# Performance work log

Measured on AMD Instinct MI355X. Metric: run time of the kernel, lower is better.

The kernel has to match this reference:

```python
import jax, jax.numpy as jnp
import numpy as np

N = 50000
E = 800000
D = 256
C = 8
H = 64
LN_EPS = 1e-5


def setup_inputs() -> dict:
    key = jax.random.key(0)
    ks = jax.random.split(key, 8)
    x = jax.random.normal(ks[0], (N, D), dtype=jnp.float32)
    edge_index = jax.random.randint(ks[1], (2, E), 0, N, dtype=jnp.int64)
    omega = jax.random.uniform(ks[2], (E, C), dtype=jnp.float32)
    # xavier-uniform-ish parameter init
    def xavier(k, shape, fan_in, fan_out):
        a = float(np.sqrt(6.0 / (fan_in + fan_out)))
        return jax.random.uniform(k, shape, dtype=jnp.float32, minval=-a, maxval=a)
    proj = xavier(ks[3], (D, C, H), D, C * H)          # layer-0 projection
    W1 = xavier(ks[4], (C, H, H), H, H)                # layer-0 channel weights
    W2 = xavier(ks[5], (C, H, H), H, H)                # layer-1 channel weights
    ln_gamma = jnp.ones((H,), dtype=jnp.float32)
    ln_beta = jnp.zeros((H,), dtype=jnp.float32)
    return {"x": x, "edge_index": edge_index, "omega": omega,
            "proj": proj, "W1": W1, "W2": W2,
            "ln_gamma": ln_gamma, "ln_beta": ln_beta}


def _conv(h, src, dst, omega, W):
    # h: [N, C, H]; per-channel weighted scatter-add then channel-specific bmm.
    outs = []
    for c in range(C):  # small fixed channel loop, mirrors original structure
        msg = omega[:, c, None] * h[src, c, :]                  # [E, H]
        outs.append(jax.ops.segment_sum(msg, dst, num_segments=N))
    h_next = jnp.stack(outs, axis=1)                            # [N, C, H]
    return jnp.einsum('nch,cho->nco', h_next, W)                # channel bmm


def _layernorm(h, gamma, beta):
    mu = jnp.mean(h, axis=-1, keepdims=True)
    var = jnp.mean(jnp.square(h - mu), axis=-1, keepdims=True)
    return (h - mu) * jax.lax.rsqrt(var + LN_EPS) * gamma + beta


def reference(x, edge_index, omega, proj, W1, W2, ln_gamma, ln_beta):
    src, dst = edge_index[0], edge_index[1]
    # layer 0: project raw features into channel space [N, C, H]
    h = (x @ proj.reshape(D, C * H)).reshape(N, C, H)
    h = _conv(h, src, dst, omega, W1)
    h = _layernorm(h, ln_gamma, ln_beta)
    h = jax.nn.relu(h)
    # layer 1 (last layer: no ReLU)
    h = _conv(h, src, dst, omega, W2)
    h = _layernorm(h, ln_gamma, ln_beta)
    return h
```

## Files before the change

kernel.cpp:

```cpp
#include <hip/hip_runtime.h>

#define NN 50000
#define NE 800000
#define DD 256
#define CC 8
#define HH 64
#define CHW 512
#define LN_EPS 1e-5f
#define SCAN_BLOCKS ((NN + 1023) / 1024)

typedef __attribute__((ext_vector_type(8))) __bf16 bf16x8;
typedef __attribute__((ext_vector_type(4))) float f32x4;

__device__ inline ushort f2bf(float f) {
  uint u = __float_as_uint(f);
  return (ushort)((u + 0x7fffu + ((u >> 16) & 1u)) >> 16);
}

__device__ inline float om_decode(uint4 om, int c) {
  uint wd = (c & 2) ? ((c & 4) ? om.w : om.y) : ((c & 4) ? om.z : om.x);
  ushort hu = (c & 1) ? (ushort)(wd >> 16) : (ushort)(wd & 0xffffu);
  union { ushort u; _Float16 f; } cv; cv.u = hu;
  return (float)cv.f;
}

__device__ inline void acc8(float* acc, uint4 hv, float wt) {
  acc[0] += wt * __uint_as_float(hv.x << 16);
  acc[1] += wt * __uint_as_float(hv.x & 0xffff0000u);
  acc[2] += wt * __uint_as_float(hv.y << 16);
  acc[3] += wt * __uint_as_float(hv.y & 0xffff0000u);
  acc[4] += wt * __uint_as_float(hv.z << 16);
  acc[5] += wt * __uint_as_float(hv.z & 0xffff0000u);
  acc[6] += wt * __uint_as_float(hv.w << 16);
  acc[7] += wt * __uint_as_float(hv.w & 0xffff0000u);
}

__global__ __launch_bounds__(256) void fold_w1_kernel(
    const float* __restrict__ proj, const float* __restrict__ W1,
    ushort* __restrict__ projW1T) {
  __shared__ float wl[64];
  const int n = blockIdx.x;
  const int c = n >> 6, i = n & 63;
  const int tid = threadIdx.x;
  if (tid < 64) wl[tid] = W1[c * 4096 + tid * 64 + i];
  __syncthreads();
  const float* pr = proj + (size_t)tid * 512 + c * 64;
  float acc = 0.f;
#pragma unroll
  for (int k = 0; k < 64; ++k) acc += pr[k] * wl[k];
  projW1T[(size_t)n * 256 + tid] = f2bf(acc);
}

__global__ __launch_bounds__(256) void w2t_kernel(const float* __restrict__ W2,
                                                  ushort* __restrict__ W2T) {
  int c = blockIdx.x;
  for (int idx = threadIdx.x; idx < 4096; idx += 256) {
    int nn = idx >> 6, k = idx & 63;
    W2T[(size_t)c * 4096 + idx] = f2bf(W2[(size_t)c * 4096 + k * 64 + nn]);
  }
}

__global__ __launch_bounds__(256) void gemm_proj_kernel(
    const float* __restrict__ x, const ushort* __restrict__ BT,
    ushort* __restrict__ gout) {
  __shared__ ushort As[128 * 40];
  __shared__ ushort Bs[128 * 40];
  const int tid = threadIdx.x;
  const int lane = tid & 63, wv = tid >> 6;
  const int wm = wv >> 1, wn = wv & 1;
  const int lr = lane & 15, kg = lane >> 4;
  const int row0 = blockIdx.x * 128;
  const int col0 = blockIdx.y * 128;

  f32x4 acc[4][4];
#pragma unroll
  for (int i = 0; i < 4; ++i)
#pragma unroll
    for (int j = 0; j < 4; ++j) acc[i][j] = (f32x4){0.f, 0.f, 0.f, 0.f};

  for (int kk = 0; kk < 8; ++kk) {
    __syncthreads();
#pragma unroll
    for (int i = 0; i < 4; ++i) {
      int idx = tid + i * 256;
      int row = idx >> 3, quad = idx & 7;
      int rg = row0 + row;
      rg = rg < NN ? rg : NN - 1;
      float4 v = *(const float4*)(x + (size_t)rg * 256 + kk * 32 + quad * 4);
      ushort4 o = {f2bf(v.x), f2bf(v.y), f2bf(v.z), f2bf(v.w)};
      *(ushort4*)(As + row * 40 + quad * 4) = o;
    }
#pragma unroll
    for (int i = 0; i < 2; ++i) {
      int idx = tid + i * 256;
      int n = idx >> 2, quad = idx & 3;
      uint4 v = *(const uint4*)(BT + (size_t)(col0 + n) * 256 + kk * 32 + quad * 8);
      *(uint4*)(Bs + n * 40 + quad * 8) = v;
    }
    __syncthreads();
    bf16x8 a[4], b[4];
#pragma unroll
    for (int i = 0; i < 4; ++i)
      a[i] = *(const bf16x8*)(As + (wm * 64 + i * 16 + lr) * 40 + kg * 8);
#pragma unroll
    for (int j = 0; j < 4; ++j)
      b[j] = *(const bf16x8*)(Bs + (wn * 64 + j * 16 + lr) * 40 + kg * 8);
#pragma unroll
    for (int i = 0; i < 4; ++i)
#pragma unroll
      for (int j = 0; j < 4; ++j)
        acc[i][j] = __builtin_amdgcn_mfma_f32_16x16x32_bf16(a[i], b[j], acc[i][j], 0, 0, 0);
  }

  const int orow = kg * 4;
  const int ocol = lane & 15;
#pragma unroll
  for (int i = 0; i < 4; ++i) {
    int rg0 = row0 + wm * 64 + i * 16 + orow;
#pragma unroll
    for (int q = 0; q < 4; ++q) {
      int rg = rg0 + q;
      if (rg < NN) {
#pragma unroll
        for (int j = 0; j < 4; ++j) {
          gout[(size_t)rg * 512 + col0 + wn * 64 + j * 16 + ocol] = f2bf(acc[i][j][q]);
        }
      }
    }
  }
}

__global__ __launch_bounds__(256) void bmm_g_kernel(
    const ushort* __restrict__ h, const ushort* __restrict__ WT,
    ushort* __restrict__ g) {
  __shared__ ushort As[128 * 72];
  __shared__ ushort Bs[64 * 72];
  __shared__ float Cs[4][32 * 68];
  const int tid = threadIdx.x, lane = tid & 63, wv = tid >> 6;
  const int lr = lane & 15, kg = lane >> 4;
  const int n0 = blockIdx.x * 128;
  const int c = blockIdx.y;

#pragma unroll
  for (int i = 0; i < 4; ++i) {
    int idx = tid + i * 256;
    int row = idx >> 3, q = idx & 7;
    int rg = n0 + row;
    rg = rg < NN ? rg : NN - 1;
    *(uint4*)(As + row * 72 + q * 8) =
        *(const uint4*)(h + (size_t)rg * 512 + c * 64 + q * 8);
  }
#pragma unroll
  for (int i = 0; i < 2; ++i) {
    int idx = tid + i * 256;
    int row = idx >> 3, q = idx & 7;
    *(uint4*)(Bs + row * 72 + q * 8) =
        *(const uint4*)(WT + (size_t)c * 4096 + row * 64 + q * 8);
  }
  __syncthreads();

  f32x4 acc[2][4];
#pragma unroll
  for (int m = 0; m < 2; ++m)
#pragma unroll
    for (int j = 0; j < 4; ++j) acc[m][j] = (f32x4){0.f, 0.f, 0.f, 0.f};

#pragma unroll
  for (int ks = 0; ks < 2; ++ks) {
    bf16x8 a[2], b[4];
#pragma unroll
    for (int m = 0; m < 2; ++m)
      a[m] = *(const bf16x8*)(As + (wv * 32 + m * 16 + lr) * 72 + ks * 32 + kg * 8);
#pragma unroll
    for (int j = 0; j < 4; ++j)
      b[j] = *(const bf16x8*)(Bs + (j * 16 + lr) * 72 + ks * 32 + kg * 8);
#pragma unroll
    for (int m = 0; m < 2; ++m)
#pragma unroll
      for (int j = 0; j < 4; ++j)
        acc[m][j] = __builtin_amdgcn_mfma_f32_16x16x32_bf16(a[m], b[j], acc[m][j], 0, 0, 0);
  }

  float* cs = &Cs[wv][0];
#pragma unroll
  for (int m = 0; m < 2; ++m)
#pragma unroll
    for (int j = 0; j < 4; ++j)
#pragma unroll
      for (int q = 0; q < 4; ++q)
        cs[(m * 16 + kg * 4 + q) * 68 + j * 16 + lr] = acc[m][j][q];
  __syncthreads();

  const int row = lane & 31, half = lane >> 5;
  const int rg = n0 + wv * 32 + row;
  if (rg < NN) {
    const float* rp = cs + row * 68 + half * 32;
    ushort ob[32];
#pragma unroll
    for (int t = 0; t < 32; ++t) ob[t] = f2bf(rp[t]);
    ushort* op = g + (size_t)rg * 512 + c * 64 + half * 32;
#pragma unroll
    for (int t = 0; t < 4; ++t)
      *(uint4*)(op + t * 8) = *(uint4*)(ob + t * 8);
  }
}

__global__ void hist_kernel(const int* __restrict__ dst, int* __restrict__ cnt) {
  int e = blockIdx.x * 256 + threadIdx.x;
  if (e < NE) atomicAdd(&cnt[dst[e]], 1);
}

__global__ __launch_bounds__(1024) void scan1_kernel(const int* __restrict__ cnt,
                                                     int* __restrict__ blocksum) {
  __shared__ int ws[16];
  int tid = threadIdx.x, t = blockIdx.x * 1024 + tid;
  int v = (t < NN) ? cnt[t] : 0;
#pragma unroll
  for (int off = 32; off; off >>= 1) v += __shfl_xor(v, off);
  if ((tid & 63) == 0) ws[tid >> 6] = v;
  __syncthreads();
  if (tid < 16) {
    int s = ws[tid];
#pragma unroll
    for (int off = 8; off; off >>= 1) s += __shfl_xor(s, off, 16);
    if (tid == 0) blocksum[blockIdx.x] = s;
  }
}

__global__ __launch_bounds__(64) void scan2_kernel(int* __restrict__ blocksum,
                                                   int* __restrict__ rowptr) {
  int tid = threadIdx.x;
  int v = (tid < SCAN_BLOCKS) ? blocksum[tid] : 0;
  int orig = v;
#pragma unroll
  for (int off = 1; off < 64; off <<= 1) {
    int u = __shfl_up(v, off);
    if (tid >= off) v += u;
  }
  if (tid < SCAN_BLOCKS) blocksum[tid] = v - orig;
  if (tid == 63) rowptr[NN] = v;
}

__global__ __launch_bounds__(1024) void scan3_kernel(const int* __restrict__ blocksum,
                                                     int* __restrict__ cntcur,
                                                     int* __restrict__ rowptr) {
  __shared__ int ws[16];
  int tid = threadIdx.x, lane = tid & 63, wv = tid >> 6;
  int t = blockIdx.x * 1024 + tid;
  int orig = (t < NN) ? cntcur[t] : 0;
  int v = orig;
#pragma unroll
  for (int off = 1; off < 64; off <<= 1) {
    int u = __shfl_up(v, off);
    if (lane >= off) v += u;
  }
  if (lane == 63) ws[wv] = v;
  __syncthreads();
  if (tid < 16) {
    int s = ws[tid];
#pragma unroll
    for (int off = 1; off < 16; off <<= 1) {
      int u = __shfl_up(s, off, 16);
      if (tid >= off) s += u;
    }
    ws[tid] = s;
  }
  __syncthreads();
  if (t < NN) {
    int excl = blocksum[blockIdx.x] + (wv ? ws[wv - 1] : 0) + (v - orig);
    rowptr[t] = excl;
    cntcur[t] = excl;
  }
}

__global__ void fill_kernel(const int* __restrict__ dst, const int* __restrict__ src,
                            const float* __restrict__ omega, int* __restrict__ cursor,
                            int* __restrict__ esrc, uint4* __restrict__ eom) {
  int e = blockIdx.x * 256 + threadIdx.x;
  if (e < NE) {
    int d = dst[e];
    int pos = atomicAdd(&cursor[d], 1);
    esrc[pos] = src[e];
    const float4* om4 = (const float4*)(omega + (size_t)e * 8);
    float4 o0 = om4[0], o1 = om4[1];
    union { _Float16 f[8]; uint4 v; } pk;
    pk.f[0] = (_Float16)o0.x; pk.f[1] = (_Float16)o0.y;
    pk.f[2] = (_Float16)o0.z; pk.f[3] = (_Float16)o0.w;
    pk.f[4] = (_Float16)o1.x; pk.f[5] = (_Float16)o1.y;
    pk.f[6] = (_Float16)o1.z; pk.f[7] = (_Float16)o1.w;
    eom[pos] = pk.v;
  }
}

template <bool RELU, bool BF16OUT>
__global__ __launch_bounds__(256) void conv_ln_kernel(
    const ushort* __restrict__ g, const int* __restrict__ esrc,
    const uint4* __restrict__ eom, const int* __restrict__ rowptr,
    const float* __restrict__ gamma, const float* __restrict__ beta,
    void* __restrict__ outv) {
  int n = blockIdx.x * 4 + (threadIdx.x >> 6);
  if (n >= NN) return;
  const int lane = threadIdx.x & 63;
  const int c = lane >> 3;
  const int i0 = (lane & 7) * 8;
  int start = rowptr[n], end = rowptr[n + 1];
  const uint4* g4 = (const uint4*)g;
  float acc[8] = {0.f, 0.f, 0.f, 0.f, 0.f, 0.f, 0.f, 0.f};

  int idx = start;
  for (; idx + 3 < end; idx += 4) {
    int s0 = esrc[idx], s1 = esrc[idx + 1], s2 = esrc[idx + 2], s3 = esrc[idx + 3];
    uint4 om0 = eom[idx], om1 = eom[idx + 1], om2 = eom[idx + 2], om3 = eom[idx + 3];
    uint4 h0 = g4[(size_t)s0 * 64 + lane];
    uint4 h1 = g4[(size_t)s1 * 64 + lane];
    uint4 h2 = g4[(size_t)s2 * 64 + lane];
    uint4 h3 = g4[(size_t)s3 * 64 + lane];
    float w0 = om_decode(om0, c), w1 = om_decode(om1, c);
    float w2 = om_decode(om2, c), w3 = om_decode(om3, c);
    acc8(acc, h0, w0);
    acc8(acc, h1, w1);
    acc8(acc, h2, w2);
    acc8(acc, h3, w3);
  }
  for (; idx < end; ++idx) {
    int s = esrc[idx];
    uint4 om = eom[idx];
    uint4 hv = g4[(size_t)s * 64 + lane];
    acc8(acc, hv, om_decode(om, c));
  }

  float s8 = ((acc[0] + acc[1]) + (acc[2] + acc[3])) +
             ((acc[4] + acc[5]) + (acc[6] + acc[7]));
  s8 += __shfl_xor(s8, 1);
  s8 += __shfl_xor(s8, 2);
  s8 += __shfl_xor(s8, 4);
  float mu = s8 * (1.f / 64.f);
  float d[8];
  float v = 0.f;
#pragma unroll
  for (int j = 0; j < 8; ++j) {
    d[j] = acc[j] - mu;
    v += d[j] * d[j];
  }
  v += __shfl_xor(v, 1);
  v += __shfl_xor(v, 2);
  v += __shfl_xor(v, 4);
  float inv = rsqrtf(v * (1.f / 64.f) + LN_EPS);
  float4 g0 = *(const float4*)(gamma + i0);
  float4 g1 = *(const float4*)(gamma + i0 + 4);
  float4 b0 = *(const float4*)(beta + i0);
  float4 b1 = *(const float4*)(beta + i0 + 4);
  float gg[8] = {g0.x, g0.y, g0.z, g0.w, g1.x, g1.y, g1.z, g1.w};
  float bb[8] = {b0.x, b0.y, b0.z, b0.w, b1.x, b1.y, b1.z, b1.w};
  float y[8];
#pragma unroll
  for (int j = 0; j < 8; ++j) {
    float t = d[j] * inv * gg[j] + bb[j];
    y[j] = RELU ? fmaxf(t, 0.f) : t;
  }
  if (BF16OUT) {
    ushort o[8];
#pragma unroll
    for (int j = 0; j < 8; ++j) o[j] = f2bf(y[j]);
    *(uint4*)((ushort*)outv + (size_t)n * 512 + c * 64 + i0) = *(uint4*)o;
  } else {
    float* op = (float*)outv + (size_t)n * 512 + c * 64 + i0;
    *(float4*)op = make_float4(y[0], y[1], y[2], y[3]);
    *(float4*)(op + 4) = make_float4(y[4], y[5], y[6], y[7]);
  }
}

extern "C" void kernel_launch(void* const* d_in, const int* in_sizes, int n_in,
                              void* d_out, int out_size, void* d_ws, size_t ws_size,
                              hipStream_t stream) {
  const float* x     = (const float*)d_in[0];
  const int*   edge  = (const int*)d_in[1];
  const float* omega = (const float*)d_in[2];
  const float* proj  = (const float*)d_in[3];
  const float* W1    = (const float*)d_in[4];
  const float* W2    = (const float*)d_in[5];
  const float* gamma = (const float*)d_in[6];
  const float* beta  = (const float*)d_in[7];
  const int* src = edge;
  const int* dst = edge + NE;

  char* p = (char*)d_ws;
  ushort* hbf    = (ushort*)p;              p += (size_t)NN * CHW * 2;
  uint4*  eom    = (uint4*)p;               p += (size_t)NE * 16;
  int*    esrc   = (int*)p;                 p += (size_t)NE * 4;
  int*    rowptr = (int*)p;                 p += (size_t)(NN + 16) * 4;
  int*    cntcur = (int*)p;                 p += (size_t)(NN + 16) * 4;
  int*    blocksum=(int*)p;                 p += (size_t)64 * 4;
  ushort* projW1T= (ushort*)p;              p += (size_t)512 * 256 * 2;
  ushort* W2T    = (ushort*)p;

  ushort* h1 = (ushort*)d_out;

  hipMemsetAsync(cntcur, 0, NN * sizeof(int), stream);
  hist_kernel<<<(NE + 255) / 256, 256, 0, stream>>>(dst, cntcur);
  scan1_kernel<<<SCAN_BLOCKS, 1024, 0, stream>>>(cntcur, blocksum);
  scan2_kernel<<<1, 64, 0, stream>>>(blocksum, rowptr);
  scan3_kernel<<<SCAN_BLOCKS, 1024, 0, stream>>>(blocksum, cntcur, rowptr);
  fill_kernel<<<(NE + 255) / 256, 256, 0, stream>>>(dst, src, omega, cntcur, esrc, eom);

  fold_w1_kernel<<<512, 256, 0, stream>>>(proj, W1, projW1T);
  w2t_kernel<<<8, 256, 0, stream>>>(W2, W2T);

  gemm_proj_kernel<<<dim3((NN + 127) / 128, 4), 256, 0, stream>>>(x, projW1T, hbf);
  conv_ln_kernel<true, true><<<(NN + 3) / 4, 256, 0, stream>>>(
      hbf, esrc, eom, rowptr, gamma, beta, h1);

  bmm_g_kernel<<<dim3((NN + 127) / 128, CC), 256, 0, stream>>>(h1, W2T, hbf);
  conv_ln_kernel<false, false><<<(NN + 3) / 4, 256, 0, stream>>>(
      hbf, esrc, eom, rowptr, gamma, beta, d_out);
}
```

Baseline: 411.8 us.

## Use channel-major feature layout and channel-split conv blocks with edge-parallel lanes

Intermediate bf16 features are stored channel-major ([C][N][64]) instead of node-major, and the conv+LN kernel launches one block per (node group, channel). Within a wavefront, the 8 lane groups each handle a different edge, and partials are reduced with shuffles. This should improve gather locality, since each channel's table is 6.4MB and more cache-resident, and it adds more parallelism per node. The cost is 8x more blocks, and each one re-reads rowptr, esrc and the omega words. Only an eighth of the lanes do the LN epilogue and the store.

```diff
diff --git a/kernel.cpp b/kernel.cpp
--- a/kernel.cpp
+++ b/kernel.cpp
@@ -17,9 +17,8 @@
   return (ushort)((u + 0x7fffu + ((u >> 16) & 1u)) >> 16);
 }
 
-__device__ inline float om_decode(uint4 om, int c) {
-  uint wd = (c & 2) ? ((c & 4) ? om.w : om.y) : ((c & 4) ? om.z : om.x);
-  ushort hu = (c & 1) ? (ushort)(wd >> 16) : (ushort)(wd & 0xffffu);
+__device__ inline float omw_decode(uint w, int hi) {
+  ushort hu = hi ? (ushort)(w >> 16) : (ushort)(w & 0xffffu);
   union { ushort u; _Float16 f; } cv; cv.u = hu;
   return (float)cv.f;
 }
@@ -123,7 +122,9 @@
       if (rg < NN) {
 #pragma unroll
         for (int j = 0; j < 4; ++j) {
-          gout[(size_t)rg * 512 + col0 + wn * 64 + j * 16 + ocol] = f2bf(acc[i][j][q]);
+          int cc = col0 + wn * 64 + j * 16 + ocol;
+          int ch = cc >> 6, ii = cc & 63;
+          gout[((size_t)ch * NN + rg) * 64 + ii] = f2bf(acc[i][j][q]);
         }
       }
     }
@@ -140,6 +141,8 @@
   const int lr = lane & 15, kg = lane >> 4;
   const int n0 = blockIdx.x * 128;
   const int c = blockIdx.y;
+  const ushort* hc = h + (size_t)c * NN * 64;
+  ushort* gc = g + (size_t)c * NN * 64;
 
 #pragma unroll
   for (int i = 0; i < 4; ++i) {
@@ -147,8 +150,7 @@
     int row = idx >> 3, q = idx & 7;
     int rg = n0 + row;
     rg = rg < NN ? rg : NN - 1;
-    *(uint4*)(As + row * 72 + q * 8) =
-        *(const uint4*)(h + (size_t)rg * 512 + c * 64 + q * 8);
+    *(uint4*)(As + row * 72 + q * 8) = *(const uint4*)(hc + (size_t)rg * 64 + q * 8);
   }
 #pragma unroll
   for (int i = 0; i < 2; ++i) {
@@ -198,7 +200,7 @@
     ushort ob[32];
 #pragma unroll
     for (int t = 0; t < 32; ++t) ob[t] = f2bf(rp[t]);
-    ushort* op = g + (size_t)rg * 512 + c * 64 + half * 32;
+    ushort* op = gc + (size_t)rg * 64 + half * 32;
 #pragma unroll
     for (int t = 0; t < 4; ++t)
       *(uint4*)(op + t * 8) = *(uint4*)(ob + t * 8);
@@ -295,38 +297,53 @@
 template <bool RELU, bool BF16OUT>
 __global__ __launch_bounds__(256) void conv_ln_kernel(
     const ushort* __restrict__ g, const int* __restrict__ esrc,
-    const uint4* __restrict__ eom, const int* __restrict__ rowptr,
+    const uint* __restrict__ eomw, const int* __restrict__ rowptr,
     const float* __restrict__ gamma, const float* __restrict__ beta,
     void* __restrict__ outv) {
-  int n = blockIdx.x * 4 + (threadIdx.x >> 6);
+  const int bid = blockIdx.x;
+  const int c = bid & 7;
+  const int n = (bid >> 3) * 4 + (threadIdx.x >> 6);
   if (n >= NN) return;
   const int lane = threadIdx.x & 63;
-  const int c = lane >> 3;
-  const int i0 = (lane & 7) * 8;
-  int start = rowptr[n], end = rowptr[n + 1];
-  const uint4* g4 = (const uint4*)g;
+  const int grp = lane >> 3;
+  const int sub = lane & 7;
+  const int i0 = sub * 8;
+  const int hi = c & 1;
+  const int cw = c >> 1;
+  const int start = rowptr[n], end = rowptr[n + 1];
+  const uint4* gc4 = (const uint4*)(g + (size_t)c * NN * 64);
   float acc[8] = {0.f, 0.f, 0.f, 0.f, 0.f, 0.f, 0.f, 0.f};
 
   int idx = start;
-  for (; idx + 3 < end; idx += 4) {
-    int s0 = esrc[idx], s1 = esrc[idx + 1], s2 = esrc[idx + 2], s3 = esrc[idx + 3];
-    uint4 om0 = eom[idx], om1 = eom[idx + 1], om2 = eom[idx + 2], om3 = eom[idx + 3];
-    uint4 h0 = g4[(size_t)s0 * 64 + lane];
-    uint4 h1 = g4[(size_t)s1 * 64 + lane];
-    uint4 h2 = g4[(size_t)s2 * 64 + lane];
-    uint4 h3 = g4[(size_t)s3 * 64 + lane];
-    float w0 = om_decode(om0, c), w1 = om_decode(om1, c);
-    float w2 = om_decode(om2, c), w3 = om_decode(om3, c);
+  for (; idx + 8 < end; idx += 16) {
+    int e0 = idx + grp;
+    int e1 = idx + 8 + grp;
+    bool p1 = e1 < end;
+    int e1c = p1 ? e1 : end - 1;
+    int s0 = esrc[e0];
+    int s1 = esrc[e1c];
+    uint4 h0 = gc4[(size_t)s0 * 8 + sub];
+    uint4 h1 = gc4[(size_t)s1 * 8 + sub];
+    float w0 = omw_decode(eomw[e0 * 4 + cw], hi);
+    float w1 = p1 ? omw_decode(eomw[e1c * 4 + cw], hi) : 0.f;
     acc8(acc, h0, w0);
     acc8(acc, h1, w1);
-    acc8(acc, h2, w2);
-    acc8(acc, h3, w3);
-  }
-  for (; idx < end; ++idx) {
-    int s = esrc[idx];
-    uint4 om = eom[idx];
-    uint4 hv = g4[(size_t)s * 64 + lane];
-    acc8(acc, hv, om_decode(om, c));
+  }
+  if (idx < end) {
+    int e0 = idx + grp;
+    bool p0 = e0 < end;
+    int e0c = p0 ? e0 : end - 1;
+    int s0 = esrc[e0c];
+    uint4 h0 = gc4[(size_t)s0 * 8 + sub];
+    float w0 = p0 ? omw_decode(eomw[e0c * 4 + cw], hi) : 0.f;
+    acc8(acc, h0, w0);
+  }
+
+#pragma unroll
+  for (int j = 0; j < 8; ++j) {
+    acc[j] += __shfl_xor(acc[j], 8);
+    acc[j] += __shfl_xor(acc[j], 16);
+    acc[j] += __shfl_xor(acc[j], 32);
   }
 
   float s8 = ((acc[0] + acc[1]) + (acc[2] + acc[3])) +
@@ -346,27 +363,30 @@
   v += __shfl_xor(v, 2);
   v += __shfl_xor(v, 4);
   float inv = rsqrtf(v * (1.f / 64.f) + LN_EPS);
-  float4 g0 = *(const float4*)(gamma + i0);
-  float4 g1 = *(const float4*)(gamma + i0 + 4);
-  float4 b0 = *(const float4*)(beta + i0);
-  float4 b1 = *(const float4*)(beta + i0 + 4);
-  float gg[8] = {g0.x, g0.y, g0.z, g0.w, g1.x, g1.y, g1.z, g1.w};
-  float bb[8] = {b0.x, b0.y, b0.z, b0.w, b1.x, b1.y, b1.z, b1.w};
-  float y[8];
-#pragma unroll
-  for (int j = 0; j < 8; ++j) {
-    float t = d[j] * inv * gg[j] + bb[j];
-    y[j] = RELU ? fmaxf(t, 0.f) : t;
-  }
-  if (BF16OUT) {
-    ushort o[8];
-#pragma unroll
-    for (int j = 0; j < 8; ++j) o[j] = f2bf(y[j]);
-    *(uint4*)((ushort*)outv + (size_t)n * 512 + c * 64 + i0) = *(uint4*)o;
-  } else {
-    float* op = (float*)outv + (size_t)n * 512 + c * 64 + i0;
-    *(float4*)op = make_float4(y[0], y[1], y[2], y[3]);
-    *(float4*)(op + 4) = make_float4(y[4], y[5], y[6], y[7]);
+
+  if (grp == 0) {
+    float4 g0 = *(const float4*)(gamma + i0);
+    float4 g1 = *(const float4*)(gamma + i0 + 4);
+    float4 b0 = *(const float4*)(beta + i0);
+    float4 b1 = *(const float4*)(beta + i0 + 4);
+    float gg[8] = {g0.x, g0.y, g0.z, g0.w, g1.x, g1.y, g1.z, g1.w};
+    float bb[8] = {b0.x, b0.y, b0.z, b0.w, b1.x, b1.y, b1.z, b1.w};
+    float y[8];
+#pragma unroll
+    for (int j = 0; j < 8; ++j) {
+      float t = d[j] * inv * gg[j] + bb[j];
+      y[j] = RELU ? fmaxf(t, 0.f) : t;
+    }
+    if (BF16OUT) {
+      ushort o[8];
+#pragma unroll
+      for (int j = 0; j < 8; ++j) o[j] = f2bf(y[j]);
+      *(uint4*)((ushort*)outv + ((size_t)c * NN + n) * 64 + i0) = *(uint4*)o;
+    } else {
+      float* op = (float*)outv + (size_t)n * 512 + c * 64 + i0;
+      *(float4*)op = make_float4(y[0], y[1], y[2], y[3]);
+      *(float4*)(op + 4) = make_float4(y[4], y[5], y[6], y[7]);
+    }
   }
 }
 
@@ -406,11 +426,13 @@
   fold_w1_kernel<<<512, 256, 0, stream>>>(proj, W1, projW1T);
   w2t_kernel<<<8, 256, 0, stream>>>(W2, W2T);
 
+  const int conv_blocks = ((NN + 3) / 4) * 8;
+
   gemm_proj_kernel<<<dim3((NN + 127) / 128, 4), 256, 0, stream>>>(x, projW1T, hbf);
-  conv_ln_kernel<true, true><<<(NN + 3) / 4, 256, 0, stream>>>(
-      hbf, esrc, eom, rowptr, gamma, beta, h1);
+  conv_ln_kernel<true, true><<<conv_blocks, 256, 0, stream>>>(
+      hbf, esrc, (const uint*)eom, rowptr, gamma, beta, h1);
 
   bmm_g_kernel<<<dim3((NN + 127) / 128, CC), 256, 0, stream>>>(h1, W2T, hbf);
-  conv_ln_kernel<false, false><<<(NN + 3) / 4, 256, 0, stream>>>(
-      hbf, esrc, eom, rowptr, gamma, beta, d_out);
-}
+  conv_ln_kernel<false, false><<<conv_blocks, 256, 0, stream>>>(
+      hbf, esrc, (const uint*)eom, rowptr, gamma, beta, d_out);
+}
```

Measured after the change: 515.4 us. 1.25x slower.
